# Kernel optimization log

Hardware: AMD Instinct MI355X
Metric: run time of the kernel (lower is better)

The kernel has to match this reference:

```python
import jax, jax.numpy as jnp
import numpy as np
import math

B, L, CH, H, NL, N2 = 32, 4096, 1, 256, 4, 32  # batch, seq, channels, d_model, n_layers, d_state//2
LN_EPS = 1e-5


def setup_inputs() -> dict:
    key = jax.random.key(0)
    ks = jax.random.split(key, 12)
    rn = lambda k, shape, s=1.0: (jax.random.normal(k, shape, dtype=jnp.float32) * s)
    inp = {}
    inp["x"] = rn(ks[0], (B, L, CH))
    inp["enc_w"] = rn(ks[1], (H, CH), 1.0 / math.sqrt(CH))
    inp["enc_b"] = jnp.zeros((H,), jnp.float32)
    # S4D kernel parameters, stacked over layers (standard S4D init)
    dt_min, dt_max = 1e-3, 1e-1
    u = jax.random.uniform(ks[2], (NL, H))
    inp["log_dt"] = (u * (math.log(dt_max) - math.log(dt_min)) + math.log(dt_min)).astype(jnp.float32)
    inp["log_A_real"] = jnp.full((NL, H, N2), math.log(0.5), jnp.float32)
    inp["A_imag"] = jnp.broadcast_to(math.pi * jnp.arange(N2, dtype=jnp.float32), (NL, H, N2)) + jnp.zeros((NL, H, N2), jnp.float32)
    inp["C_re"] = rn(ks[3], (NL, H, N2))
    inp["C_im"] = rn(ks[4], (NL, H, N2))
    inp["D"] = rn(ks[5], (NL, H))
    # output_linear: 1x1 Conv1d H->2H followed by GLU
    inp["glu_w"] = rn(ks[6], (NL, 2 * H, H), 1.0 / math.sqrt(H))
    inp["glu_b"] = jnp.zeros((NL, 2 * H), jnp.float32)
    inp["ln_g"] = jnp.ones((NL, H), jnp.float32)
    inp["ln_b"] = jnp.zeros((NL, H), jnp.float32)
    inp["dec1_w"] = rn(ks[7], (1, L), 1.0 / math.sqrt(L))
    inp["dec1_b"] = jnp.zeros((1,), jnp.float32)
    inp["dec2_w"] = rn(ks[8], (1, H), 1.0 / math.sqrt(H))
    inp["dec2_b"] = jnp.zeros((1,), jnp.float32)
    return inp


def _s4d_layer(u_bhl, log_dt, log_A_real, A_imag, C_re, C_im, D, glu_w, glu_b):
    """S4D block on (B, H, L): FFT conv with diagonal-SSM kernel + skip D + GELU + GLU output linear."""
    Lx = u_bhl.shape[-1]
    dt = jnp.exp(log_dt)                          # (H,)
    A = -jnp.exp(log_A_real) + 1j * A_imag        # (H, N2) complex
    C = C_re + 1j * C_im                          # (H, N2)
    dtA = A * dt[:, None]                         # (H, N2)
    Ck = C * (jnp.exp(dtA) - 1.0) / A             # ZOH-style discretized C
    # Vandermonde kernel: k[h, l] = 2 * Re( sum_n Ck[h,n] * exp(dtA[h,n] * l) )
    expdtA = jnp.exp(dtA[:, :, None] * jnp.arange(Lx, dtype=jnp.float32))  # (H, N2, L)
    k = 2.0 * jnp.einsum('hn,hnl->hl', Ck, expdtA).real                    # (H, L)
    # causal conv via zero-padded FFT
    kf = jnp.fft.rfft(k, n=2 * Lx)
    uf = jnp.fft.rfft(u_bhl, n=2 * Lx)
    y = jnp.fft.irfft(uf * kf, n=2 * Lx)[..., :Lx]
    y = y + u_bhl * D[:, None]
    y = jax.nn.gelu(y, approximate=False)
    # 1x1 conv H -> 2H, then GLU over the channel dim
    y = jnp.einsum('oh,bhl->bol', glu_w, y) + glu_b[:, None]
    a, g = jnp.split(y, 2, axis=-2)
    return a * jax.nn.sigmoid(g)


def reference(x, enc_w, enc_b, log_dt, log_A_real, A_imag, C_re, C_im, D,
              glu_w, glu_b, ln_g, ln_b, dec1_w, dec1_b, dec2_w, dec2_b):
    h = x @ enc_w.T + enc_b                 # (B, L, H)
    h = jnp.swapaxes(h, -1, -2)             # (B, H, L)
    for i in range(NL):
        z = _s4d_layer(h, log_dt[i], log_A_real[i], A_imag[i], C_re[i], C_im[i],
                       D[i], glu_w[i], glu_b[i])
        h = z + h                           # residual (dropout = identity in eval)
        ht = jnp.swapaxes(h, -1, -2)        # (B, L, H) -> LayerNorm over H (postnorm)
        mu = ht.mean(-1, keepdims=True)
        var = ht.var(-1, keepdims=True)
        ht = (ht - mu) / jnp.sqrt(var + LN_EPS) * ln_g[i] + ln_b[i]
        h = jnp.swapaxes(ht, -1, -2)
    y = jnp.einsum('bhl,ol->bho', h, dec1_w) + dec1_b   # (B, H, 1)
    y = y.squeeze(-1)                                    # (B, H)
    y = y @ dec2_w.T + dec2_b                            # (B, 1)
    y = y.squeeze(-1)                                    # (B,)
    return jax.nn.sigmoid(y)
```

## Files before the change

kernel.cpp:

```cpp
#include <hip/hip_runtime.h>
#include <math.h>

#define WS_WT   16777216
#define WS_Y1   17039360
#define WS_A256 17047552
#define WS_V    17063936
#define WS_ABUF 19161088
#define WS_S    29646848

typedef unsigned short ushort_t;
struct __attribute__((aligned(8))) us4 { ushort_t x, y, z, w; };
typedef short bf16x8 __attribute__((ext_vector_type(8)));
typedef float f32x4  __attribute__((ext_vector_type(4)));

__device__ __forceinline__ float bf2f(ushort_t u) {
    union { unsigned int i; float f; } c; c.i = ((unsigned int)u) << 16; return c.f;
}
__device__ __forceinline__ ushort_t f2bf(float f) {
    union { float f; unsigned int i; } c; c.f = f;
    unsigned int x = c.i;
    unsigned int r = (x + 0x7FFF + ((x >> 16) & 1)) >> 16;
    return (ushort_t)r;
}
__device__ __forceinline__ float fast_gelu(float v) {
    float y = 1.5957691216057308f * (v + 0.044715f * v * v * v);
    return v / (1.f + __expf(-y));
}

__global__ __launch_bounds__(256) void enc_kernel(const float* __restrict__ x,
    const float* __restrict__ ew, const float* __restrict__ eb, ushort_t* __restrict__ Hb)
{
    int i = blockIdx.x * 256 + threadIdx.x;
    int l8 = i & 511;
    int h  = (i >> 9) & 255;
    int b  = i >> 17;
    const float* xp = x + ((size_t)b << 12) + (l8 << 3);
    float4 a0 = ((const float4*)xp)[0];
    float4 a1 = ((const float4*)xp)[1];
    float w = ew[h], bb = eb[h];
    us4 o0, o1;
    o0.x = f2bf(fmaf(a0.x, w, bb)); o0.y = f2bf(fmaf(a0.y, w, bb));
    o0.z = f2bf(fmaf(a0.z, w, bb)); o0.w = f2bf(fmaf(a0.w, w, bb));
    o1.x = f2bf(fmaf(a1.x, w, bb)); o1.y = f2bf(fmaf(a1.y, w, bb));
    o1.z = f2bf(fmaf(a1.z, w, bb)); o1.w = f2bf(fmaf(a1.w, w, bb));
    us4* op = (us4*)(Hb + ((size_t)i << 3));
    op[0] = o0; op[1] = o1;
}

__global__ __launch_bounds__(256) void wtb_kernel(const float* __restrict__ gw, ushort_t* __restrict__ wTb)
{
    int i = blockIdx.x * 256 + threadIdx.x;
    wTb[i] = f2bf(gw[i]);
}

__global__ __launch_bounds__(256) void prep_kernel(
    const float* __restrict__ log_dt, const float* __restrict__ lAr,
    const float* __restrict__ Aim_, const float* __restrict__ Cre,
    const float* __restrict__ Cim, ushort_t* __restrict__ Abuf,
    ushort_t* __restrict__ Vg, float* __restrict__ a256tab, int li)
{
    __shared__ float s_ar[32], s_ai[32], s_ckr[32], s_cki[32];
    __shared__ float powr[8][32], powi[8][32];
    __shared__ ushort_t kb[256];
    __shared__ ushort_t Vt[256][66];
    __shared__ ushort_t Wt[256][66];
    int t = threadIdx.x;
    int h = blockIdx.x;
    int pb = (li * 256 + h) * 32;

    if (t < 32) {
        int s = t;
        float dt = expf(log_dt[li * 256 + h]);
        float Are = -expf(lAr[pb + s]);
        float Ai  = Aim_[pb + s];
        float e = expf(Are * dt);
        float ar = e * cosf(Ai * dt), ai = e * sinf(Ai * dt);
        float inv = 1.f / (Are * Are + Ai * Ai);
        float numr = ar - 1.f, numi = ai;
        float tr = (numr * Are + numi * Ai) * inv;
        float ti = (numi * Are - numr * Ai) * inv;
        float cr = Cre[pb + s], ci = Cim[pb + s];
        s_ar[s] = ar; s_ai[s] = ai;
        s_ckr[s] = 2.f * (cr * tr - ci * ti);
        s_cki[s] = 2.f * (cr * ti + ci * tr);
        float xr = ar, xi = ai;
        for (int k = 0; k < 8; k++) {
            powr[k][s] = xr; powi[k][s] = xi;
            float nr = xr * xr - xi * xi;
            float ni = 2.f * xr * xi;
            xr = nr; xi = ni;
        }
        a256tab[h * 64 + s * 2] = xr;
        a256tab[h * 64 + s * 2 + 1] = xi;
    }
    __syncthreads();

    int d = t;
    float adr[32], adi[32];
    #pragma unroll
    for (int s = 0; s < 32; s++) { adr[s] = 1.f; adi[s] = 0.f; }
    #pragma unroll
    for (int bit = 0; bit < 8; bit++) {
        if (d & (1 << bit)) {
            #pragma unroll
            for (int s = 0; s < 32; s++) {
                float pr_ = powr[bit][s], pi_ = powi[bit][s];
                float nr = adr[s] * pr_ - adi[s] * pi_;
                float ni = adr[s] * pi_ + adi[s] * pr_;
                adr[s] = nr; adi[s] = ni;
            }
        }
    }
    float kd = 0.f;
    #pragma unroll
    for (int s = 0; s < 32; s++) kd += s_ckr[s] * adr[s] - s_cki[s] * adi[s];
    kb[d] = f2bf(kd);
    #pragma unroll
    for (int s = 0; s < 32; s++) {
        float wr = adr[s] * s_ar[s] - adi[s] * s_ai[s];
        float wi = adr[s] * s_ai[s] + adi[s] * s_ar[s];
        float v0 = s_ckr[s] * wr - s_cki[s] * wi;
        float v1 = -(s_ckr[s] * wi + s_cki[s] * wr);
        *(unsigned int*)&Wt[d][2 * s] =
            (unsigned int)f2bf(v0) | ((unsigned int)f2bf(v1) << 16);
    }
    {
        int e = 255 - d;
        float evr[32], evi[32];
        #pragma unroll
        for (int s = 0; s < 32; s++) { evr[s] = 1.f; evi[s] = 0.f; }
        #pragma unroll
        for (int bit = 0; bit < 8; bit++) {
            if (e & (1 << bit)) {
                #pragma unroll
                for (int s = 0; s < 32; s++) {
                    float pr_ = powr[bit][s], pi_ = powi[bit][s];
                    float nr = evr[s] * pr_ - evi[s] * pi_;
                    float ni = evr[s] * pi_ + evi[s] * pr_;
                    evr[s] = nr; evi[s] = ni;
                }
            }
        }
        #pragma unroll
        for (int s = 0; s < 32; s++) {
            Vt[d][2*s]   = f2bf(evr[s]);
            Vt[d][2*s+1] = f2bf(evi[s]);
        }
    }
    __syncthreads();

    {
        ushort_t* Ab = Abuf + (size_t)h * 81920;
        #pragma unroll 4
        for (int i = 0; i < 80; i++) {
            int f = i * 256 + t;
            int row = f / 80;
            int cq = f - row * 80;
            int col = cq * 4;
            us4 v;
            if (col < 256) {
                int idx = row - col;
                v.x = (idx >= 0) ? kb[idx]     : (ushort_t)0;
                v.y = (idx >= 1) ? kb[idx - 1] : (ushort_t)0;
                v.z = (idx >= 2) ? kb[idx - 2] : (ushort_t)0;
                v.w = (idx >= 3) ? kb[idx - 3] : (ushort_t)0;
            } else {
                int wc = col - 256;
                v.x = Wt[row][wc]; v.y = Wt[row][wc + 1];
                v.z = Wt[row][wc + 2]; v.w = Wt[row][wc + 3];
            }
            *(us4*)(Ab + (size_t)f * 4) = v;
        }
    }
    {
        int m = t >> 2, jq = t & 3;
        ushort_t* vrow = Vg + (size_t)h * 16384 + (size_t)m * 256 + jq * 64;
        for (int j4 = 0; j4 < 16; j4++) {
            int j = jq * 64 + j4 * 4;
            us4 v;
            v.x = Vt[j][m]; v.y = Vt[j+1][m]; v.z = Vt[j+2][m]; v.w = Vt[j+3][m];
            *(us4*)(vrow + j4 * 4) = v;
        }
    }
}

__global__ __launch_bounds__(256, 2) void s4df_kernel(
    const ushort_t* __restrict__ U, const ushort_t* __restrict__ Abuf,
    const ushort_t* __restrict__ Vg, const float* __restrict__ a256tab,
    const float* __restrict__ Dp, ushort_t* __restrict__ G, int li, int b0)
{
    __shared__ ushort_t yt[64 * 320];
    __shared__ ushort_t sS[64 * 66];
    int t = threadIdx.x;
    int h = blockIdx.x;
    int tile = blockIdx.y;
    int nl = t & 63, kq = t >> 6;
    int n = tile * 64 + nl;
    int sw = nl & 7;
    const ushort_t* ub = U + (size_t)(b0 + (n >> 4)) * 1048576 + (size_t)h * 4096 + (n & 15) * 256;
    #pragma unroll
    for (int i = 0; i < 8; i++) {
        int c = kq * 8 + i;
        *(uint4*)(&yt[nl * 320 + ((c ^ sw) << 3)]) = *(const uint4*)(ub + c * 8);
    }
    __syncthreads();

    int lane = t & 63, w = t >> 6;
    int ln15 = lane & 15, quad = lane >> 4;
    int rsw = ln15 & 7;

    {
        const ushort_t* va = Vg + (size_t)h * 16384 + (size_t)(w * 16 + ln15) * 256;
        f32x4 acc[4] = {};
        bf16x8 vab[2];
        vab[0] = *(const bf16x8*)(va + quad * 8);
        #pragma unroll
        for (int ks = 0; ks < 8; ks++) {
            int cur = ks & 1;
            if (ks < 7) vab[cur ^ 1] = *(const bf16x8*)(va + (ks + 1) * 32 + quad * 8);
            int c = ks * 4 + quad;
            #pragma unroll
            for (int nt = 0; nt < 4; nt++) {
                bf16x8 bf_ = *(const bf16x8*)(&yt[(nt * 16 + ln15) * 320 + ((c ^ rsw) << 3)]);
                acc[nt] = __builtin_amdgcn_mfma_f32_16x16x32_bf16(vab[cur], bf_, acc[nt], 0, 0, 0);
            }
        }
        #pragma unroll
        for (int nt = 0; nt < 4; nt++) {
            int m = w * 16 + quad * 4;
            int nn = nt * 16 + ln15;
            sS[(m    ) * 66 + nn] = f2bf(acc[nt][0]);
            sS[(m + 1) * 66 + nn] = f2bf(acc[nt][1]);
            sS[(m + 2) * 66 + nn] = f2bf(acc[nt][2]);
            sS[(m + 3) * 66 + nn] = f2bf(acc[nt][3]);
        }
    }
    __syncthreads();

    if (t < 128) {
        int bq = t >> 5, s = t & 31;
        float m2r = a256tab[h * 64 + s * 2], m2i = a256tab[h * 64 + s * 2 + 1];
        int col = 256 + 2 * s;
        int cc = col >> 3, off = col & 7;
        float sr = 0.f, si = 0.f;
        for (int c = 0; c < 16; c++) {
            int nn = bq * 16 + c;
            float Sr = bf2f(sS[(2 * s) * 66 + nn]);
            float Si = bf2f(sS[(2 * s + 1) * 66 + nn]);
            int addr = nn * 320 + ((cc ^ (nn & 7)) << 3) + off;
            yt[addr] = f2bf(sr);
            yt[addr + 1] = f2bf(si);
            float nsr = m2r * sr - m2i * si + Sr;
            float nsi = m2r * si + m2i * sr + Si;
            sr = nsr; si = nsi;
        }
    }
    __syncthreads();

    const ushort_t* Ah = Abuf + (size_t)h * 81920 + (size_t)(w * 64 + ln15) * 320 + quad * 8;
    f32x4 acc[4][4] = {};
    bf16x8 afb[2][4];
    #pragma unroll
    for (int mt = 0; mt < 4; mt++)
        afb[0][mt] = *(const bf16x8*)(Ah + (size_t)(mt * 16) * 320);
    #pragma unroll
    for (int ks = 0; ks < 10; ks++) {
        int cur = ks & 1;
        if (ks < 9) {
            #pragma unroll
            for (int mt = 0; mt < 4; mt++)
                afb[cur ^ 1][mt] = *(const bf16x8*)(Ah + (size_t)(mt * 16) * 320 + (ks + 1) * 32);
        }
        int c = ks * 4 + quad;
        #pragma unroll
        for (int nt = 0; nt < 4; nt++) {
            bf16x8 bf_ = *(const bf16x8*)(&yt[(nt * 16 + ln15) * 320 + ((c ^ rsw) << 3)]);
            #pragma unroll
            for (int mt = 0; mt < 4; mt++)
                acc[mt][nt] = __builtin_amdgcn_mfma_f32_16x16x32_bf16(afb[cur][mt], bf_, acc[mt][nt], 0, 0, 0);
        }
    }
    float Dh = Dp[li * 256 + h];
    #pragma unroll
    for (int mt = 0; mt < 4; mt++) {
        #pragma unroll
        for (int nt = 0; nt < 4; nt++) {
            int nn = tile * 64 + nt * 16 + ln15;
            int lb = w * 64 + mt * 16 + quad * 4;
            int c = lb >> 3, co = lb & 7;
            us4 uv = *(const us4*)(&yt[(nt * 16 + ln15) * 320 + ((c ^ rsw) << 3) + co]);
            float uu[4] = {bf2f(uv.x), bf2f(uv.y), bf2f(uv.z), bf2f(uv.w)};
            us4 o;
            ushort_t* op = &o.x;
            #pragma unroll
            for (int rr = 0; rr < 4; rr++) {
                float v = acc[mt][nt][rr] + Dh * uu[rr];
                op[rr] = f2bf(fast_gelu(v));
            }
            ushort_t* gp = G + ((size_t)(nn >> 4) * 256 + h) * 4096 + (nn & 15) * 256 + lb;
            *(us4*)gp = o;
        }
    }
}

#define LDK 268
__global__ __launch_bounds__(256, 2) void gluln_kernel(
    const ushort_t* __restrict__ G, const ushort_t* __restrict__ wTb,
    const float* __restrict__ glu_b, const float* __restrict__ ln_g,
    const float* __restrict__ ln_b, ushort_t* __restrict__ Hb, int li, int b0)
{
    __shared__ ushort_t yt[64 * LDK];
    __shared__ float sred[4][64], sqred[4][64];
    __shared__ float mup[64], rstd[64];
    int t = threadIdx.x;
    int pf = blockIdx.x * 64;
    int bloc = pf >> 12;
    int l0 = pf & 4095;
    int b = b0 + bloc;

    const ushort_t* gb = G + (size_t)bloc * 1048576 + l0;
    unsigned int* dst = (unsigned int*)&yt[0];
    #pragma unroll
    for (int i = 0; i < 4; i++) {
        int hp = ((i & 1) << 6) + (t >> 2);
        int pg = ((i >> 1) << 2) + (t & 3);
        int h0 = hp * 2;
        uint4 va = *(const uint4*)(gb + (size_t)h0 * 4096 + pg * 8);
        uint4 vb = *(const uint4*)(gb + (size_t)(h0 + 1) * 4096 + pg * 8);
        const ushort_t* ra = (const ushort_t*)&va;
        const ushort_t* rb = (const ushort_t*)&vb;
        #pragma unroll
        for (int j = 0; j < 8; j++) {
            unsigned int v = (unsigned int)ra[j] | ((unsigned int)rb[j] << 16);
            dst[(pg * 8 + j) * (LDK / 2) + hp] = v;
        }
    }
    __syncthreads();

    int lane = t & 63, w = t >> 6;
    int ln15 = lane & 15, quad = lane >> 4;
    int oA = w * 64;
    const ushort_t* wA = wTb + li * 131072;

    f32x4 accA[4][4] = {};
    f32x4 accG[4][4] = {};

    for (int ks = 0; ks < 8; ks++) {
        int kk = ks * 32 + quad * 8;
        bf16x8 af[4], gf[4];
        #pragma unroll
        for (int mt = 0; mt < 4; mt++) {
            int oa = oA + mt * 16 + ln15;
            af[mt] = *(const bf16x8*)(wA + (size_t)oa * 256 + kk);
            gf[mt] = *(const bf16x8*)(wA + (size_t)(oa + 256) * 256 + kk);
        }
        bf16x8 bfr[4];
        #pragma unroll
        for (int nt = 0; nt < 4; nt++) {
            const us4* yp = (const us4*)&yt[(nt * 16 + ln15) * LDK + kk];
            us4 lo = yp[0], hi = yp[1];
            bf16x8 v;
            v[0] = (short)lo.x; v[1] = (short)lo.y; v[2] = (short)lo.z; v[3] = (short)lo.w;
            v[4] = (short)hi.x; v[5] = (short)hi.y; v[6] = (short)hi.z; v[7] = (short)hi.w;
            bfr[nt] = v;
        }
        #pragma unroll
        for (int mt = 0; mt < 4; mt++)
            #pragma unroll
            for (int nt = 0; nt < 4; nt++) {
                accA[mt][nt] = __builtin_amdgcn_mfma_f32_16x16x32_bf16(bfr[nt], af[mt], accA[mt][nt], 0, 0, 0);
                accG[mt][nt] = __builtin_amdgcn_mfma_f32_16x16x32_bf16(bfr[nt], gf[mt], accG[mt][nt], 0, 0, 0);
            }
    }

    ushort_t* hb_ = Hb + (size_t)b * 1048576;
    us4 hold[4][4];
    #pragma unroll
    for (int mt = 0; mt < 4; mt++) {
        const ushort_t* hrow = hb_ + (size_t)(oA + mt * 16 + ln15) * 4096 + l0 + quad * 4;
        #pragma unroll
        for (int nt = 0; nt < 4; nt++)
            hold[mt][nt] = *(const us4*)(hrow + nt * 16);
    }

    float ba[4], bg[4];
    #pragma unroll
    for (int mt = 0; mt < 4; mt++) {
        int o = oA + mt * 16 + ln15;
        ba[mt] = glu_b[li * 512 + o];
        bg[mt] = glu_b[li * 512 + 256 + o];
    }

    float psl[4][4] = {}, pql[4][4] = {};
    #pragma unroll
    for (int mt = 0; mt < 4; mt++) {
        #pragma unroll
        for (int nt = 0; nt < 4; nt++) {
            const ushort_t* hp4 = &hold[mt][nt].x;
            #pragma unroll
            for (int r = 0; r < 4; r++) {
                float a = accA[mt][nt][r] + ba[mt];
                float g = accG[mt][nt][r] + bg[mt];
                float z = a / (1.f + __expf(-g));
                float hn = z + bf2f(hp4[r]);
                accA[mt][nt][r] = hn;
                psl[nt][r] += hn; pql[nt][r] = fmaf(hn, hn, pql[nt][r]);
            }
        }
    }
    #pragma unroll
    for (int nt = 0; nt < 4; nt++)
        #pragma unroll
        for (int r = 0; r < 4; r++) {
            float s = psl[nt][r], q = pql[nt][r];
            s += __shfl_xor(s, 1, 64); q += __shfl_xor(q, 1, 64);
            s += __shfl_xor(s, 2, 64); q += __shfl_xor(q, 2, 64);
            s += __shfl_xor(s, 4, 64); q += __shfl_xor(q, 4, 64);
            s += __shfl_xor(s, 8, 64); q += __shfl_xor(q, 8, 64);
            psl[nt][r] = s; pql[nt][r] = q;
        }
    if (ln15 == 0) {
        #pragma unroll
        for (int nt = 0; nt < 4; nt++)
            #pragma unroll
            for (int r = 0; r < 4; r++) {
                int p = nt * 16 + quad * 4 + r;
                sred[w][p] = psl[nt][r];
                sqred[w][p] = pql[nt][r];
            }
    }
    __syncthreads();
    if (t < 64) {
        float S = (sred[0][t] + sred[1][t]) + (sred[2][t] + sred[3][t]);
        float Q = (sqred[0][t] + sqred[1][t]) + (sqred[2][t] + sqred[3][t]);
        float mu = S * (1.f / 256.f);
        float var = Q * (1.f / 256.f) - mu * mu;
        mup[t] = mu; rstd[t] = rsqrtf(var + 1e-5f);
    }
    __syncthreads();

    #pragma unroll
    for (int mt = 0; mt < 4; mt++) {
        int o = oA + mt * 16 + ln15;
        float gm = ln_g[li * 256 + o];
        float bt = ln_b[li * 256 + o];
        ushort_t* hrow = hb_ + (size_t)o * 4096 + l0 + quad * 4;
        #pragma unroll
        for (int nt = 0; nt < 4; nt++) {
            us4 ov;
            ushort_t* op = &ov.x;
            #pragma unroll
            for (int r = 0; r < 4; r++) {
                int p = nt * 16 + quad * 4 + r;
                float v = (accA[mt][nt][r] - mup[p]) * rstd[p] * gm + bt;
                op[r] = f2bf(v);
            }
            *(us4*)(hrow + nt * 16) = ov;
        }
    }
}

__global__ __launch_bounds__(256) void dec1_kernel(const ushort_t* __restrict__ Hb,
    const float* __restrict__ w1, const float* __restrict__ b1, float* __restrict__ y1)
{
    int bh = blockIdx.x;
    const ushort_t* base = Hb + (size_t)bh * 4096;
    int t = threadIdx.x;
    float s = 0.f;
    for (int l = t; l < 4096; l += 256) s = fmaf(bf2f(base[l]), w1[l], s);
    #pragma unroll
    for (int d = 32; d > 0; d >>= 1) s += __shfl_xor(s, d, 64);
    __shared__ float red[4];
    if ((t & 63) == 0) red[t >> 6] = s;
    __syncthreads();
    if (t == 0) y1[bh] = red[0] + red[1] + red[2] + red[3] + b1[0];
}

__global__ __launch_bounds__(256) void dec2_kernel(const float* __restrict__ y1,
    const float* __restrict__ w2, const float* __restrict__ b2, float* __restrict__ out)
{
    int t = threadIdx.x;
    int b = blockIdx.x * 4 + (t >> 6);
    int lane = t & 63;
    float s = 0.f;
    #pragma unroll
    for (int k = 0; k < 4; k++) s = fmaf(y1[b * 256 + lane + k * 64], w2[lane + k * 64], s);
    #pragma unroll
    for (int d = 32; d > 0; d >>= 1) s += __shfl_xor(s, d, 64);
    if (lane == 0) out[b] = 1.f / (1.f + expf(-(s + b2[0])));
}

extern "C" void kernel_launch(void* const* d_in, const int* in_sizes, int n_in,
                              void* d_out, int out_size, void* d_ws, size_t ws_size,
                              hipStream_t stream)
{
    const float* x      = (const float*)d_in[0];
    const float* enc_w  = (const float*)d_in[1];
    const float* enc_b  = (const float*)d_in[2];
    const float* log_dt = (const float*)d_in[3];
    const float* lAr    = (const float*)d_in[4];
    const float* Aim    = (const float*)d_in[5];
    const float* Cre    = (const float*)d_in[6];
    const float* Cim    = (const float*)d_in[7];
    const float* Dp     = (const float*)d_in[8];
    const float* glu_w  = (const float*)d_in[9];
    const float* glu_b  = (const float*)d_in[10];
    const float* ln_g   = (const float*)d_in[11];
    const float* ln_b   = (const float*)d_in[12];
    const float* w1     = (const float*)d_in[13];
    const float* b1     = (const float*)d_in[14];
    const float* w2     = (const float*)d_in[15];
    const float* b2     = (const float*)d_in[16];

    float* ws = (float*)d_ws;
    ushort_t* Hb   = (ushort_t*)ws;
    ushort_t* wTb  = (ushort_t*)(ws + WS_WT);
    float* y1      = ws + WS_Y1;
    float* a256    = ws + WS_A256;
    ushort_t* Vg   = (ushort_t*)(ws + WS_V);
    ushort_t* Abuf = (ushort_t*)(ws + WS_ABUF);
    float* outp    = (float*)d_out;

    size_t wsf = ws_size / 4;
    int nb = 32;
    while (nb > 4 && (size_t)WS_S + (size_t)nb * 655360 > wsf) nb >>= 1;
    ushort_t* Gb = (ushort_t*)(ws + WS_S + (size_t)nb * 131072);

    wtb_kernel<<<2048, 256, 0, stream>>>(glu_w, wTb);
    enc_kernel<<<16384, 256, 0, stream>>>(x, enc_w, enc_b, Hb);
    for (int li = 0; li < 4; li++) {
        prep_kernel<<<256, 256, 0, stream>>>(log_dt, lAr, Aim, Cre, Cim, Abuf, Vg, a256, li);
        for (int b0 = 0; b0 < 32; b0 += nb) {
            s4df_kernel<<<dim3(256, nb / 4), 256, 0, stream>>>(Hb, Abuf, Vg, a256, Dp, Gb, li, b0);
            gluln_kernel<<<nb * 64, 256, 0, stream>>>(Gb, wTb, glu_b, ln_g, ln_b, Hb, li, b0);
        }
    }
    dec1_kernel<<<8192, 256, 0, stream>>>(Hb, w1, b1, y1);
    dec2_kernel<<<8, 256, 0, stream>>>(y1, w2, b2, outp);
}
```

Before: 997.9 us.

## Split GLU+LayerNorm kernel across 16 waves with one output tile per wave

Raises the gluln block from 256 to 1024 threads. Each wave now computes a single 16-row output tile instead of four, which shrinks per-thread accumulator registers and spreads the tile load and LN reduction over 16 waves. The aim is more latency hiding and occupancy for this GEMM-plus-epilogue stage. The cost is a wider cross-wave reduction, more B-fragment LDS reads per wave, and less register reuse of the activation fragments.

Result: slower. 1.098 ms (+10.0%).

```diff
diff --git a/kernel.cpp b/kernel.cpp
--- a/kernel.cpp
+++ b/kernel.cpp
@@ -304,13 +304,13 @@
 }
 
 #define LDK 268
-__global__ __launch_bounds__(256, 2) void gluln_kernel(
+__global__ __launch_bounds__(1024, 4) void gluln_kernel(
     const ushort_t* __restrict__ G, const ushort_t* __restrict__ wTb,
     const float* __restrict__ glu_b, const float* __restrict__ ln_g,
     const float* __restrict__ ln_b, ushort_t* __restrict__ Hb, int li, int b0)
 {
     __shared__ ushort_t yt[64 * LDK];
-    __shared__ float sred[4][64], sqred[4][64];
+    __shared__ float sred[16][64], sqred[16][64];
     __shared__ float mup[64], rstd[64];
     int t = threadIdx.x;
     int pf = blockIdx.x * 64;
@@ -320,10 +320,9 @@
 
     const ushort_t* gb = G + (size_t)bloc * 1048576 + l0;
     unsigned int* dst = (unsigned int*)&yt[0];
-    #pragma unroll
-    for (int i = 0; i < 4; i++) {
-        int hp = ((i & 1) << 6) + (t >> 2);
-        int pg = ((i >> 1) << 2) + (t & 3);
+    {
+        int hp = t >> 3;
+        int pg = t & 7;
         int h0 = hp * 2;
         uint4 va = *(const uint4*)(gb + (size_t)h0 * 4096 + pg * 8);
         uint4 vb = *(const uint4*)(gb + (size_t)(h0 + 1) * 4096 + pg * 8);
@@ -339,22 +338,18 @@
 
     int lane = t & 63, w = t >> 6;
     int ln15 = lane & 15, quad = lane >> 4;
-    int oA = w * 64;
+    int o = w * 16 + ln15;
     const ushort_t* wA = wTb + li * 131072;
-
-    f32x4 accA[4][4] = {};
-    f32x4 accG[4][4] = {};
+    const ushort_t* wap = wA + (size_t)o * 256;
+    const ushort_t* wgp = wA + (size_t)(o + 256) * 256;
+
+    f32x4 accA[4] = {};
+    f32x4 accG[4] = {};
 
     for (int ks = 0; ks < 8; ks++) {
         int kk = ks * 32 + quad * 8;
-        bf16x8 af[4], gf[4];
-        #pragma unroll
-        for (int mt = 0; mt < 4; mt++) {
-            int oa = oA + mt * 16 + ln15;
-            af[mt] = *(const bf16x8*)(wA + (size_t)oa * 256 + kk);
-            gf[mt] = *(const bf16x8*)(wA + (size_t)(oa + 256) * 256 + kk);
-        }
-        bf16x8 bfr[4];
+        bf16x8 af = *(const bf16x8*)(wap + kk);
+        bf16x8 gf = *(const bf16x8*)(wgp + kk);
         #pragma unroll
         for (int nt = 0; nt < 4; nt++) {
             const us4* yp = (const us4*)&yt[(nt * 16 + ln15) * LDK + kk];
@@ -362,50 +357,32 @@
             bf16x8 v;
             v[0] = (short)lo.x; v[1] = (short)lo.y; v[2] = (short)lo.z; v[3] = (short)lo.w;
             v[4] = (short)hi.x; v[5] = (short)hi.y; v[6] = (short)hi.z; v[7] = (short)hi.w;
-            bfr[nt] = v;
-        }
-        #pragma unroll
-        for (int mt = 0; mt < 4; mt++)
-            #pragma unroll
-            for (int nt = 0; nt < 4; nt++) {
-                accA[mt][nt] = __builtin_amdgcn_mfma_f32_16x16x32_bf16(bfr[nt], af[mt], accA[mt][nt], 0, 0, 0);
-                accG[mt][nt] = __builtin_amdgcn_mfma_f32_16x16x32_bf16(bfr[nt], gf[mt], accG[mt][nt], 0, 0, 0);
-            }
+            accA[nt] = __builtin_amdgcn_mfma_f32_16x16x32_bf16(v, af, accA[nt], 0, 0, 0);
+            accG[nt] = __builtin_amdgcn_mfma_f32_16x16x32_bf16(v, gf, accG[nt], 0, 0, 0);
+        }
     }
 
     ushort_t* hb_ = Hb + (size_t)b * 1048576;
-    us4 hold[4][4];
-    #pragma unroll
-    for (int mt = 0; mt < 4; mt++) {
-        const ushort_t* hrow = hb_ + (size_t)(oA + mt * 16 + ln15) * 4096 + l0 + quad * 4;
-        #pragma unroll
-        for (int nt = 0; nt < 4; nt++)
-            hold[mt][nt] = *(const us4*)(hrow + nt * 16);
-    }
-
-    float ba[4], bg[4];
-    #pragma unroll
-    for (int mt = 0; mt < 4; mt++) {
-        int o = oA + mt * 16 + ln15;
-        ba[mt] = glu_b[li * 512 + o];
-        bg[mt] = glu_b[li * 512 + 256 + o];
-    }
+    const ushort_t* hrow = hb_ + (size_t)o * 4096 + l0 + quad * 4;
+    us4 hold[4];
+    #pragma unroll
+    for (int nt = 0; nt < 4; nt++) hold[nt] = *(const us4*)(hrow + nt * 16);
+
+    float bav = glu_b[li * 512 + o];
+    float bgv = glu_b[li * 512 + 256 + o];
 
     float psl[4][4] = {}, pql[4][4] = {};
     #pragma unroll
-    for (int mt = 0; mt < 4; mt++) {
-        #pragma unroll
-        for (int nt = 0; nt < 4; nt++) {
-            const ushort_t* hp4 = &hold[mt][nt].x;
-            #pragma unroll
-            for (int r = 0; r < 4; r++) {
-                float a = accA[mt][nt][r] + ba[mt];
-                float g = accG[mt][nt][r] + bg[mt];
-                float z = a / (1.f + __expf(-g));
-                float hn = z + bf2f(hp4[r]);
-                accA[mt][nt][r] = hn;
-                psl[nt][r] += hn; pql[nt][r] = fmaf(hn, hn, pql[nt][r]);
-            }
+    for (int nt = 0; nt < 4; nt++) {
+        const ushort_t* hp4 = &hold[nt].x;
+        #pragma unroll
+        for (int r = 0; r < 4; r++) {
+            float a = accA[nt][r] + bav;
+            float g = accG[nt][r] + bgv;
+            float z = a / (1.f + __expf(-g));
+            float hn = z + bf2f(hp4[r]);
+            accA[nt][r] = hn;
+            psl[nt][r] += hn; pql[nt][r] = fmaf(hn, hn, pql[nt][r]);
         }
     }
     #pragma unroll
@@ -431,20 +408,19 @@
     }
     __syncthreads();
     if (t < 64) {
-        float S = (sred[0][t] + sred[1][t]) + (sred[2][t] + sred[3][t]);
-        float Q = (sqred[0][t] + sqred[1][t]) + (sqred[2][t] + sqred[3][t]);
+        float S = 0.f, Q = 0.f;
+        #pragma unroll
+        for (int s_ = 0; s_ < 16; s_++) { S += sred[s_][t]; Q += sqred[s_][t]; }
         float mu = S * (1.f / 256.f);
         float var = Q * (1.f / 256.f) - mu * mu;
         mup[t] = mu; rstd[t] = rsqrtf(var + 1e-5f);
     }
     __syncthreads();
 
-    #pragma unroll
-    for (int mt = 0; mt < 4; mt++) {
-        int o = oA + mt * 16 + ln15;
+    {
         float gm = ln_g[li * 256 + o];
         float bt = ln_b[li * 256 + o];
-        ushort_t* hrow = hb_ + (size_t)o * 4096 + l0 + quad * 4;
+        ushort_t* hw = hb_ + (size_t)o * 4096 + l0 + quad * 4;
         #pragma unroll
         for (int nt = 0; nt < 4; nt++) {
             us4 ov;
@@ -452,10 +428,10 @@
             #pragma unroll
             for (int r = 0; r < 4; r++) {
                 int p = nt * 16 + quad * 4 + r;
-                float v = (accA[mt][nt][r] - mup[p]) * rstd[p] * gm + bt;
+                float v = (accA[nt][r] - mup[p]) * rstd[p] * gm + bt;
                 op[r] = f2bf(v);
             }
-            *(us4*)(hrow + nt * 16) = ov;
+            *(us4*)(hw + nt * 16) = ov;
         }
     }
 }
@@ -532,7 +508,7 @@
         prep_kernel<<<256, 256, 0, stream>>>(log_dt, lAr, Aim, Cre, Cim, Abuf, Vg, a256, li);
         for (int b0 = 0; b0 < 32; b0 += nb) {
             s4df_kernel<<<dim3(256, nb / 4), 256, 0, stream>>>(Hb, Abuf, Vg, a256, Dp, Gb, li, b0);
-            gluln_kernel<<<nb * 64, 256, 0, stream>>>(Gb, wTb, glu_b, ln_g, ln_b, Hb, li, b0);
+            gluln_kernel<<<nb * 64, 1024, 0, stream>>>(Gb, wTb, glu_b, ln_g, ln_b, Hb, li, b0);
         }
     }
     dec1_kernel<<<8192, 256, 0, stream>>>(Hb, w1, b1, y1);
```
